# Kernel tuning notes

Hardware: AMD Instinct MI355X
Metric: run time of the kernel (lower is better)

The kernel has to match this reference:

```python
import jax, jax.numpy as jnp
import numpy as np

B, S, D, H = 256, 200, 256, 4
HD = D // H
R = 16  # HIE reduced rank (hardcoded in module)
EPS = 1e-12


def setup_inputs() -> dict:
    key = jax.random.key(0)
    ks = jax.random.split(key, 32)
    w = lambda k, sh: jax.random.normal(k, sh, jnp.float32) * 0.02
    inp = {
        'input_tensor': jax.random.normal(ks[0], (B, S, D), jnp.float32),
        'fusion_tensor': jax.random.normal(ks[1], (B, S, D), jnp.float32),
        'pos_tensor': jax.random.normal(ks[2], (B, S, D), jnp.float32),
        'attention_mask': jnp.zeros((B, 1, 1, S), jnp.float32),
        # projections (stored as (in, out); apply as x @ W + b)
        'Wv': w(ks[3], (D, D)), 'bv': w(ks[4], (D,)),
        'Wqf': w(ks[5], (D, D)), 'bqf': w(ks[6], (D,)),
        'Wkf': w(ks[7], (D, D)), 'bkf': w(ks[8], (D,)),
        'Wvf': w(ks[9], (D, D)), 'bvf': w(ks[10], (D,)),
        'Wqp': w(ks[11], (D, D)), 'bqp': w(ks[12], (D,)),
        'Wkp': w(ks[13], (D, D)), 'bkp': w(ks[14], (D,)),
        'Wvp': w(ks[15], (D, D)), 'bvp': w(ks[16], (D,)),
        # output dense + LayerNorm per branch
        'Wd': w(ks[17], (D, D)), 'bd': w(ks[18], (D,)),
        'g1': jnp.ones((D,), jnp.float32), 'b1': jnp.zeros((D,), jnp.float32),
        'Wfd': w(ks[19], (D, D)), 'bfd': w(ks[20], (D,)),
        'g2': jnp.ones((D,), jnp.float32), 'b2': jnp.zeros((D,), jnp.float32),
        'Wpd': w(ks[21], (D, D)), 'bpd': w(ks[22], (D,)),
        'g3': jnp.ones((D,), jnp.float32), 'b3': jnp.zeros((D,), jnp.float32),
        # HIE parameter (n, r)
        'Wr': jax.random.normal(ks[23], (S, R), jnp.float32),
    }
    return inp


def _heads(t):
    # (B,S,D) -> (B,H,S,HD)
    return t.reshape(B, S, H, HD).transpose(0, 2, 1, 3)


def _layernorm(x, g, b):
    m = jnp.mean(x, axis=-1, keepdims=True)
    v = jnp.mean((x - m) ** 2, axis=-1, keepdims=True)
    return (x - m) * jax.lax.rsqrt(v + EPS) * g + b


def _compute(resid, value_layer, scores, mask, Wd, bd, g, b):
    s = scores / np.sqrt(HD) + mask
    probs = jax.nn.softmax(s, axis=-1)  # (attn dropout = identity in eval)
    ctx = jnp.einsum('bhqk,bhkd->bhqd', probs, value_layer)
    ctx = ctx.transpose(0, 2, 1, 3).reshape(B, S, D)
    return _layernorm(ctx @ Wd + bd + resid, g, b)


def _hie(hX, hA, Wr):
    # reduce sequence dim, batched QR on (d, r) columns
    hr = jnp.einsum('bnd,nr->brd', hX, Wr)        # (B,R,D)
    Q, _ = jnp.linalg.qr(hr.transpose(0, 2, 1))   # (B,D,R), reduced
    pX = hX @ Q                                    # (B,S,R)
    pA = hA @ Q
    pAt = (pX * pA > 0).astype(pA.dtype) * pA      # indicator gate
    return jnp.einsum('bnr,bdr->bnd', pAt, Q)


def reference(input_tensor, fusion_tensor, pos_tensor, attention_mask,
              Wv, bv, Wqf, bqf, Wkf, bkf, Wvf, bvf, Wqp, bqp, Wkp, bkp,
              Wvp, bvp, Wd, bd, g1, b1, Wfd, bfd, g2, b2, Wpd, bpd, g3, b3, Wr):
    item_v = _heads(input_tensor @ Wv + bv)
    fq = _heads(fusion_tensor @ Wqf + bqf)
    fk = _heads(fusion_tensor @ Wkf + bkf)
    fv = _heads(fusion_tensor @ Wvf + bvf)
    pq = _heads(pos_tensor @ Wqp + bqp)
    pk = _heads(pos_tensor @ Wkp + bkp)
    pv = _heads(pos_tensor @ Wvp + bvp)

    item_scores = jnp.einsum('bhqd,bhkd->bhqk', fq, fk)
    pos_scores = jnp.einsum('bhqd,bhkd->bhqk', pq, pk)
    both_scores = item_scores + pos_scores

    h = _compute(input_tensor, item_v, both_scores, attention_mask, Wd, bd, g1, b1)
    hf = _compute(fusion_tensor, fv, item_scores, attention_mask, Wfd, bfd, g2, b2)
    hp = _compute(pos_tensor, pv, pos_scores, attention_mask, Wpd, bpd, g3, b3)

    h = h + _hie(h, hf, Wr)
    return (h, hf, hp)
```

## Files before the change

kernel.cpp:

```cpp
#include <hip/hip_runtime.h>


constexpr int B_ = 256, S_ = 200, D_ = 256, H_ = 4, R_ = 16;
constexpr int M_ = B_ * S_;
constexpr size_t BSD = (size_t)B_ * S_ * D_;

typedef __attribute__((ext_vector_type(8))) short bf16x8;
typedef __attribute__((ext_vector_type(4))) short bf16x4;
typedef __attribute__((ext_vector_type(4))) float f32x4;

#if __has_builtin(__builtin_amdgcn_mfma_f32_16x16x16bf16_1k)
#define MFMA16(A, B, C) __builtin_amdgcn_mfma_f32_16x16x16bf16_1k((A), (B), (C), 0, 0, 0)
#define HAVE_MFMA16 1
#else
#define HAVE_MFMA16 0
#endif

__device__ __forceinline__ float bf2f(unsigned short u) {
  union { unsigned int i; float f; } v; v.i = ((unsigned int)u) << 16; return v.f;
}
__device__ __forceinline__ unsigned short f2bf_rne(float f) {
  union { float f; unsigned int i; } v; v.f = f;
  unsigned int u = v.i;
  u += 0x7FFFu + ((u >> 16) & 1u);
  return (unsigned short)(u >> 16);
}
__device__ __forceinline__ void split8(const float* v, bf16x8& hi, bf16x8& lo) {
#pragma unroll
  for (int i = 0; i < 8; ++i) {
    unsigned short h = f2bf_rne(v[i]);
    hi[i] = (short)h;
    lo[i] = (short)f2bf_rne(v[i] - bf2f(h));
  }
}
__device__ __forceinline__ void unpack8(uint4 a, uint4 b, bf16x8& hi, bf16x8& lo) {
  union { bf16x8 v; unsigned int u[4]; } H, L;
  H.u[0] = (a.x & 0xffffu) | (a.y << 16);
  H.u[1] = (a.z & 0xffffu) | (a.w << 16);
  H.u[2] = (b.x & 0xffffu) | (b.y << 16);
  H.u[3] = (b.z & 0xffffu) | (b.w << 16);
  L.u[0] = (a.x >> 16) | (a.y & 0xffff0000u);
  L.u[1] = (a.z >> 16) | (a.w & 0xffff0000u);
  L.u[2] = (b.x >> 16) | (b.y & 0xffff0000u);
  L.u[3] = (b.z >> 16) | (b.w & 0xffff0000u);
  hi = H.v; lo = L.v;
}

struct GemmArgs {
  const float* X[7]; const float* bias[7]; float* Y[7];
  const float* resid[7]; const float* g[7]; const float* bvec[7];
  const unsigned short* stash;
};
struct WSplitArgs { const float* W[7]; };

__global__ __launch_bounds__(256) void split_w(WSplitArgs wa, unsigned short* stash)
{
  const int z = blockIdx.y;
  const int idx = blockIdx.x * 256 + threadIdx.x;
  const int k = idx >> 8, n = idx & 255;
  const float x = wa.W[z][idx];
  const unsigned short h = f2bf_rne(x);
  const unsigned short l = f2bf_rne(x - bf2f(h));
  const size_t o = (size_t)z * 131072 + (size_t)n * 256 + k;
  stash[o] = h;
  stash[o + 65536] = l;
}

template<int MODE>
__global__ __launch_bounds__(256, 2) void gemm_mfma(GemmArgs ga)
{
  __shared__ unsigned short lds[30720];
  unsigned short* Ah = lds;
  unsigned short* Al = Ah + 128 * 40;
  unsigned short* Bh = Al + 128 * 40;
  unsigned short* Bl = Bh + 256 * 40;
  const int t = threadIdx.x;
  const int z = blockIdx.y;
  const int m0 = blockIdx.x * 128;
  const float* __restrict__ X = ga.X[z];
  const float* __restrict__ bias = ga.bias[z];
  float* __restrict__ Y = ga.Y[z];
  const unsigned short* __restrict__ Wst = ga.stash + (size_t)z * 131072;
  const int w = t >> 6, lane = t & 63;
  const int wm = w >> 1, wn = w & 1;
  const int lrow = lane & 15;
  const int lk = (lane >> 4) << 3;
  const int rsub = (lane >> 4) << 2;

  f32x4 acc[4][8];
#pragma unroll
  for (int mf = 0; mf < 4; ++mf)
#pragma unroll
    for (int nf = 0; nf < 8; ++nf)
#pragma unroll
      for (int r = 0; r < 4; ++r) acc[mf][nf][r] = 0.f;

  for (int k0 = 0; k0 < 256; k0 += 32) {
#pragma unroll
    for (int i = 0; i < 2; ++i) {
      int c = t + i * 256;
      int r = c >> 2, c8 = (c & 3) << 3;
      float xv[8];
      *reinterpret_cast<float4*>(&xv[0]) =
          *reinterpret_cast<const float4*>(X + (size_t)(m0 + r) * 256 + k0 + c8);
      *reinterpret_cast<float4*>(&xv[4]) =
          *reinterpret_cast<const float4*>(X + (size_t)(m0 + r) * 256 + k0 + c8 + 4);
      bf16x8 hv, lv;
      split8(xv, hv, lv);
      *reinterpret_cast<bf16x8*>(&Ah[r * 40 + c8]) = hv;
      *reinterpret_cast<bf16x8*>(&Al[r * 40 + c8]) = lv;
    }
#pragma unroll
    for (int i = 0; i < 4; ++i) {
      int c = t + i * 256;
      int n = c >> 2, kc = (c & 3) << 3;
      *reinterpret_cast<uint4*>(&Bh[n * 40 + kc]) =
          *reinterpret_cast<const uint4*>(Wst + (size_t)n * 256 + k0 + kc);
      *reinterpret_cast<uint4*>(&Bl[n * 40 + kc]) =
          *reinterpret_cast<const uint4*>(Wst + 65536 + (size_t)n * 256 + k0 + kc);
    }
    __syncthreads();
    bf16x8 ah[4], al[4];
#pragma unroll
    for (int mf = 0; mf < 4; ++mf) {
      int r = wm * 64 + mf * 16 + lrow;
      ah[mf] = *reinterpret_cast<const bf16x8*>(&Ah[r * 40 + lk]);
      al[mf] = *reinterpret_cast<const bf16x8*>(&Al[r * 40 + lk]);
    }
#pragma unroll
    for (int nf = 0; nf < 8; ++nf) {
      int n = wn * 128 + nf * 16 + lrow;
      bf16x8 bh = *reinterpret_cast<const bf16x8*>(&Bh[n * 40 + lk]);
      bf16x8 bl = *reinterpret_cast<const bf16x8*>(&Bl[n * 40 + lk]);
#pragma unroll
      for (int mf = 0; mf < 4; ++mf) {
        acc[mf][nf] = __builtin_amdgcn_mfma_f32_16x16x32_bf16(ah[mf], bh, acc[mf][nf], 0, 0, 0);
        acc[mf][nf] = __builtin_amdgcn_mfma_f32_16x16x32_bf16(al[mf], bh, acc[mf][nf], 0, 0, 0);
        acc[mf][nf] = __builtin_amdgcn_mfma_f32_16x16x32_bf16(ah[mf], bl, acc[mf][nf], 0, 0, 0);
      }
    }
    __syncthreads();
  }

  if (MODE == 0) {
    unsigned int* Yu = (unsigned int*)Y;
#pragma unroll
    for (int nf = 0; nf < 8; ++nf) {
      const int coln = wn * 128 + nf * 16 + lrow;
      const float bb = bias[coln];
#pragma unroll
      for (int mf = 0; mf < 4; ++mf)
#pragma unroll
        for (int r = 0; r < 4; ++r) {
          const size_t row = (size_t)(m0 + wm * 64 + mf * 16 + rsub + r);
          float v = acc[mf][nf][r] + bb;
          unsigned short hh = f2bf_rne(v);
          unsigned short ll = f2bf_rne(v - bf2f(hh));
          Yu[row * 256 + coln] = (unsigned int)hh | ((unsigned int)ll << 16);
        }
    }
  } else {
    const float* __restrict__ resid = ga.resid[z];
    const float* __restrict__ gv = ga.g[z];
    const float* __restrict__ bv = ga.bvec[z];
    float s_[4][4], q_[4][4];
#pragma unroll
    for (int mf = 0; mf < 4; ++mf)
#pragma unroll
      for (int r = 0; r < 4; ++r) { s_[mf][r] = 0.f; q_[mf][r] = 0.f; }
#pragma unroll
    for (int nf = 0; nf < 8; ++nf) {
      const int coln = wn * 128 + nf * 16 + lrow;
      const float bb = bias[coln];
#pragma unroll
      for (int mf = 0; mf < 4; ++mf)
#pragma unroll
        for (int r = 0; r < 4; ++r) {
          const size_t row = (size_t)(m0 + wm * 64 + mf * 16 + rsub + r);
          float v = acc[mf][nf][r] + bb + resid[row * 256 + coln];
          acc[mf][nf][r] = v;
          s_[mf][r] += v;
          q_[mf][r] = fmaf(v, v, q_[mf][r]);
        }
    }
#pragma unroll
    for (int mf = 0; mf < 4; ++mf)
#pragma unroll
      for (int r = 0; r < 4; ++r) {
        float sv = s_[mf][r], qv = q_[mf][r];
        sv += __shfl_xor(sv, 1); qv += __shfl_xor(qv, 1);
        sv += __shfl_xor(sv, 2); qv += __shfl_xor(qv, 2);
        sv += __shfl_xor(sv, 4); qv += __shfl_xor(qv, 4);
        sv += __shfl_xor(sv, 8); qv += __shfl_xor(qv, 8);
        s_[mf][r] = sv; q_[mf][r] = qv;
      }
    __syncthreads();
    float* red = (float*)lds;
    if (lrow == 0) {
#pragma unroll
      for (int mf = 0; mf < 4; ++mf)
#pragma unroll
        for (int r = 0; r < 4; ++r) {
          int rl = wm * 64 + mf * 16 + rsub + r;
          red[rl * 4 + wn * 2 + 0] = s_[mf][r];
          red[rl * 4 + wn * 2 + 1] = q_[mf][r];
        }
    }
    __syncthreads();
#pragma unroll
    for (int mf = 0; mf < 4; ++mf)
#pragma unroll
      for (int r = 0; r < 4; ++r) {
        int rl = wm * 64 + mf * 16 + rsub + r;
        float st = red[rl * 4 + 0] + red[rl * 4 + 2];
        float qt = red[rl * 4 + 1] + red[rl * 4 + 3];
        float mean = st * (1.0f / 256.0f);
        float var = qt * (1.0f / 256.0f) - mean * mean;
        s_[mf][r] = mean;
        q_[mf][r] = rsqrtf(var + 1e-12f);
      }
#pragma unroll
    for (int nf = 0; nf < 8; ++nf) {
      const int coln = wn * 128 + nf * 16 + lrow;
      const float gg = gv[coln], be = bv[coln];
#pragma unroll
      for (int mf = 0; mf < 4; ++mf)
#pragma unroll
        for (int r = 0; r < 4; ++r) {
          const size_t row = (size_t)(m0 + wm * 64 + mf * 16 + rsub + r);
          Y[row * 256 + coln] = (acc[mf][nf][r] - s_[mf][r]) * q_[mf][r] * gg + be;
        }
    }
  }
}

__global__ __launch_bounds__(256) void attn_mfma(
    const unsigned int* __restrict__ Qf, const unsigned int* __restrict__ Kf,
    const unsigned int* __restrict__ Qp, const unsigned int* __restrict__ Kp,
    const unsigned int* __restrict__ Vi, const unsigned int* __restrict__ Vf,
    const unsigned int* __restrict__ Vp, const float* __restrict__ mask,
    float* __restrict__ Ch, float* __restrict__ Cf, float* __restrict__ Cp)
{
  __shared__ unsigned short su[21504];
  __shared__ float mt[32];
  __shared__ float emt[32];
  constexpr int KFH = 0,     KFL = 2816,  KPH = 5632,  KPL = 8448;
  constexpr int VIH = 11264, VIL = 13824, VFH = 16384, VPH = 18944;
  const int t = threadIdx.x;
  const int mtile = blockIdx.x, h = blockIdx.y, b = blockIdx.z;
  const int w = t >> 6, lane = t & 63, lg = lane >> 4, lm = lane & 15;
  const int mbase = mtile * 128 + w * 32;
  const bool wactive = (mbase < 200);
  const size_t bh = (size_t)b * 200 * 256 + (size_t)h * 64;

  bf16x8 qfh[2][2], qfl[2][2], qph[2][2], qpl[2][2];
#pragma unroll
  for (int mf2 = 0; mf2 < 2; ++mf2) {
    int gq = mbase + mf2 * 16 + lm; if (gq > 199) gq = 199;
    const size_t qb = bh + (size_t)gq * 256;
#pragma unroll
    for (int ks = 0; ks < 2; ++ks) {
      const size_t o = qb + ks * 32 + lg * 8;
      uint4 a = *reinterpret_cast<const uint4*>(Qf + o);
      uint4 bb = *reinterpret_cast<const uint4*>(Qf + o + 4);
      unpack8(a, bb, qfh[mf2][ks], qfl[mf2][ks]);
      a = *reinterpret_cast<const uint4*>(Qp + o);
      bb = *reinterpret_cast<const uint4*>(Qp + o + 4);
      unpack8(a, bb, qph[mf2][ks], qpl[mf2][ks]);
    }
  }

  f32x4 aH[4][2], aF[4][2], aP[4][2];
#pragma unroll
  for (int df = 0; df < 4; ++df)
#pragma unroll
    for (int mf2 = 0; mf2 < 2; ++mf2)
#pragma unroll
      for (int r = 0; r < 4; ++r) { aH[df][mf2][r] = 0.f; aF[df][mf2][r] = 0.f; aP[df][mf2][r] = 0.f; }
  float lH[2] = {0.f, 0.f}, lF[2] = {0.f, 0.f}, lP[2] = {0.f, 0.f};

  for (int kt = 0; kt < 200; kt += 32) {
#pragma unroll
    for (int i = 0; i < 2; ++i) {
      int idx = t + i * 256;
      const int pk = idx >> 8;
      const int rr = (idx >> 3) & 31;
      const int c8 = (idx & 7) << 3;
      int grow = kt + rr; if (grow > 199) grow = 199;
      const unsigned int* src = pk ? Kp : Kf;
      const size_t o = bh + (size_t)grow * 256 + c8;
      uint4 a = *reinterpret_cast<const uint4*>(src + o);
      uint4 bb = *reinterpret_cast<const uint4*>(src + o + 4);
      bf16x8 hv, lv;
      unpack8(a, bb, hv, lv);
      const int KH = pk ? KPH : KFH;
      const int KL = pk ? KPL : KFL;
      *reinterpret_cast<bf16x8*>(&su[KH + rr * 88 + c8]) = hv;
      *reinterpret_cast<bf16x8*>(&su[KL + rr * 88 + c8]) = lv;
    }
#pragma unroll
    for (int i = 0; i < 2; ++i) {
      int idx = t + i * 256;
      int d = idx & 63, kv4i = (idx >> 6) << 2;
      size_t rb[4];
#pragma unroll
      for (int j = 0; j < 4; ++j) {
        int grow = kt + kv4i + j; if (grow > 199) grow = 199;
        rb[j] = bh + (size_t)grow * 256 + d;
      }
      unsigned int u0 = Vi[rb[0]], u1 = Vi[rb[1]], u2 = Vi[rb[2]], u3 = Vi[rb[3]];
      ushort4 hv, lv;
      hv.x = (unsigned short)u0; hv.y = (unsigned short)u1;
      hv.z = (unsigned short)u2; hv.w = (unsigned short)u3;
      lv.x = (unsigned short)(u0 >> 16); lv.y = (unsigned short)(u1 >> 16);
      lv.z = (unsigned short)(u2 >> 16); lv.w = (unsigned short)(u3 >> 16);
      *reinterpret_cast<ushort4*>(&su[VIH + d * 40 + kv4i]) = hv;
      *reinterpret_cast<ushort4*>(&su[VIL + d * 40 + kv4i]) = lv;
      u0 = Vf[rb[0]]; u1 = Vf[rb[1]]; u2 = Vf[rb[2]]; u3 = Vf[rb[3]];
      hv.x = (unsigned short)u0; hv.y = (unsigned short)u1;
      hv.z = (unsigned short)u2; hv.w = (unsigned short)u3;
      *reinterpret_cast<ushort4*>(&su[VFH + d * 40 + kv4i]) = hv;
      u0 = Vp[rb[0]]; u1 = Vp[rb[1]]; u2 = Vp[rb[2]]; u3 = Vp[rb[3]];
      hv.x = (unsigned short)u0; hv.y = (unsigned short)u1;
      hv.z = (unsigned short)u2; hv.w = (unsigned short)u3;
      *reinterpret_cast<ushort4*>(&su[VPH + d * 40 + kv4i]) = hv;
    }
    if (t < 32) {
      const bool valid = (kt + t < 200);
      const float mj = valid ? mask[(size_t)b * 200 + kt + t] : -1e30f;
      mt[t] = mj;
      emt[t] = valid ? __expf(-mj) : 0.f;
    }
    __syncthreads();

    if (wactive) {
      f32x4 si[2][2], sp[2][2];
#pragma unroll
      for (int kvf = 0; kvf < 2; ++kvf)
#pragma unroll
        for (int mf2 = 0; mf2 < 2; ++mf2)
#pragma unroll
          for (int r = 0; r < 4; ++r) { si[kvf][mf2][r] = 0.f; sp[kvf][mf2][r] = 0.f; }
#pragma unroll
      for (int ks = 0; ks < 2; ++ks)
#pragma unroll
        for (int kvf = 0; kvf < 2; ++kvf) {
          bf16x8 kh = *reinterpret_cast<const bf16x8*>(&su[KFH + (kvf * 16 + lm) * 88 + ks * 32 + lg * 8]);
          bf16x8 kl = *reinterpret_cast<const bf16x8*>(&su[KFL + (kvf * 16 + lm) * 88 + ks * 32 + lg * 8]);
#pragma unroll
          for (int mf2 = 0; mf2 < 2; ++mf2) {
            si[kvf][mf2] = __builtin_amdgcn_mfma_f32_16x16x32_bf16(kh, qfh[mf2][ks], si[kvf][mf2], 0, 0, 0);
            si[kvf][mf2] = __builtin_amdgcn_mfma_f32_16x16x32_bf16(kl, qfh[mf2][ks], si[kvf][mf2], 0, 0, 0);
            si[kvf][mf2] = __builtin_amdgcn_mfma_f32_16x16x32_bf16(kh, qfl[mf2][ks], si[kvf][mf2], 0, 0, 0);
          }
          kh = *reinterpret_cast<const bf16x8*>(&su[KPH + (kvf * 16 + lm) * 88 + ks * 32 + lg * 8]);
          kl = *reinterpret_cast<const bf16x8*>(&su[KPL + (kvf * 16 + lm) * 88 + ks * 32 + lg * 8]);
#pragma unroll
          for (int mf2 = 0; mf2 < 2; ++mf2) {
            sp[kvf][mf2] = __builtin_amdgcn_mfma_f32_16x16x32_bf16(kh, qph[mf2][ks], sp[kvf][mf2], 0, 0, 0);
            sp[kvf][mf2] = __builtin_amdgcn_mfma_f32_16x16x32_bf16(kl, qph[mf2][ks], sp[kvf][mf2], 0, 0, 0);
            sp[kvf][mf2] = __builtin_amdgcn_mfma_f32_16x16x32_bf16(kh, qpl[mf2][ks], sp[kvf][mf2], 0, 0, 0);
          }
        }

      f32x4 ph[2][2], pf[2][2], pp[2][2];
      float4 mv[2], ev[2];
      mv[0] = *reinterpret_cast<const float4*>(&mt[lg * 4]);
      mv[1] = *reinterpret_cast<const float4*>(&mt[16 + lg * 4]);
      ev[0] = *reinterpret_cast<const float4*>(&emt[lg * 4]);
      ev[1] = *reinterpret_cast<const float4*>(&emt[16 + lg * 4]);
#pragma unroll
      for (int kvf = 0; kvf < 2; ++kvf)
#pragma unroll
        for (int mf2 = 0; mf2 < 2; ++mf2)
#pragma unroll
          for (int r = 0; r < 4; ++r) {
            float mj = (r == 0) ? mv[kvf].x : (r == 1) ? mv[kvf].y : (r == 2) ? mv[kvf].z : mv[kvf].w;
            float ej = (r == 0) ? ev[kvf].x : (r == 1) ? ev[kvf].y : (r == 2) ? ev[kvf].z : ev[kvf].w;
            float vF = __expf(fmaf(si[kvf][mf2][r], 0.125f, mj));
            float vP = __expf(fmaf(sp[kvf][mf2][r], 0.125f, mj));
            float vH = vF * vP * ej;
            pf[kvf][mf2][r] = vF; pp[kvf][mf2][r] = vP; ph[kvf][mf2][r] = vH;
            lF[mf2] += vF; lP[mf2] += vP; lH[mf2] += vH;
          }

#if HAVE_MFMA16
#pragma unroll
      for (int kvf = 0; kvf < 2; ++kvf) {
        bf16x4 bH[2], bL[2], bF[2], bP[2];
#pragma unroll
        for (int mf2 = 0; mf2 < 2; ++mf2) {
#pragma unroll
          for (int i = 0; i < 4; ++i) {
            float vH = ph[kvf][mf2][i];
            unsigned short hh = f2bf_rne(vH);
            bH[mf2][i] = (short)hh;
            bL[mf2][i] = (short)f2bf_rne(vH - bf2f(hh));
            bF[mf2][i] = (short)f2bf_rne(pf[kvf][mf2][i]);
            bP[mf2][i] = (short)f2bf_rne(pp[kvf][mf2][i]);
          }
        }
#pragma unroll
        for (int df = 0; df < 4; ++df) {
          const int rowb = (df * 16 + lm) * 40 + kvf * 16 + lg * 4;
          bf16x4 vih = *reinterpret_cast<const bf16x4*>(&su[VIH + rowb]);
          bf16x4 vil = *reinterpret_cast<const bf16x4*>(&su[VIL + rowb]);
          bf16x4 vfh = *reinterpret_cast<const bf16x4*>(&su[VFH + rowb]);
          bf16x4 vph = *reinterpret_cast<const bf16x4*>(&su[VPH + rowb]);
#pragma unroll
          for (int mf2 = 0; mf2 < 2; ++mf2) {
            aH[df][mf2] = MFMA16(vih, bH[mf2], aH[df][mf2]);
            aH[df][mf2] = MFMA16(vil, bH[mf2], aH[df][mf2]);
            aH[df][mf2] = MFMA16(vih, bL[mf2], aH[df][mf2]);
            aF[df][mf2] = MFMA16(vfh, bF[mf2], aF[df][mf2]);
            aP[df][mf2] = MFMA16(vph, bP[mf2], aP[df][mf2]);
          }
        }
      }
#else
#define PV3(P, VH, VL, ACC)                                                    \
      {                                                                        \
        bf16x8 Bh[2], Bl[2];                                                   \
        _Pragma("unroll")                                                      \
        for (int mf2 = 0; mf2 < 2; ++mf2) {                                    \
          _Pragma("unroll")                                                    \
          for (int i = 0; i < 8; ++i) {                                        \
            int src = ((((lg & 1) * 2 + (i >> 2)) << 4) | lm);                 \
            float t0 = __shfl(P[0][mf2][i & 3], src);                          \
            float t1 = __shfl(P[1][mf2][i & 3], src);                          \
            float v = (lg < 2) ? t0 : t1;                                      \
            unsigned short hh = f2bf_rne(v);                                   \
            Bh[mf2][i] = (short)hh;                                            \
            Bl[mf2][i] = (short)f2bf_rne(v - bf2f(hh));                        \
          }                                                                    \
        }                                                                      \
        _Pragma("unroll")                                                      \
        for (int df = 0; df < 4; ++df) {                                       \
          bf16x8 vh = *reinterpret_cast<const bf16x8*>(&su[VH + (df * 16 + lm) * 40 + lg * 8]); \
          bf16x8 vl = *reinterpret_cast<const bf16x8*>(&su[VL + (df * 16 + lm) * 40 + lg * 8]); \
          _Pragma("unroll")                                                    \
          for (int mf2 = 0; mf2 < 2; ++mf2) {                                  \
            ACC[df][mf2] = __builtin_amdgcn_mfma_f32_16x16x32_bf16(vh, Bh[mf2], ACC[df][mf2], 0, 0, 0); \
            ACC[df][mf2] = __builtin_amdgcn_mfma_f32_16x16x32_bf16(vl, Bh[mf2], ACC[df][mf2], 0, 0, 0); \
            ACC[df][mf2] = __builtin_amdgcn_mfma_f32_16x16x32_bf16(vh, Bl[mf2], ACC[df][mf2], 0, 0, 0); \
          }                                                                    \
        }                                                                      \
      }
#define PV1(P, VH, ACC)                                                        \
      {                                                                        \
        bf16x8 Bh[2];                                                          \
        _Pragma("unroll")                                                      \
        for (int mf2 = 0; mf2 < 2; ++mf2) {                                    \
          _Pragma("unroll")                                                    \
          for (int i = 0; i < 8; ++i) {                                        \
            int src = ((((lg & 1) * 2 + (i >> 2)) << 4) | lm);                 \
            float t0 = __shfl(P[0][mf2][i & 3], src);                          \
            float t1 = __shfl(P[1][mf2][i & 3], src);                          \
            float v = (lg < 2) ? t0 : t1;                                      \
            Bh[mf2][i] = (short)f2bf_rne(v);                                   \
          }                                                                    \
        }                                                                      \
        _Pragma("unroll")                                                      \
        for (int df = 0; df < 4; ++df) {                                       \
          bf16x8 vh = *reinterpret_cast<const bf16x8*>(&su[VH + (df * 16 + lm) * 40 + lg * 8]); \
          _Pragma("unroll")                                                    \
          for (int mf2 = 0; mf2 < 2; ++mf2)                                    \
            ACC[df][mf2] = __builtin_amdgcn_mfma_f32_16x16x32_bf16(vh, Bh[mf2], ACC[df][mf2], 0, 0, 0); \
        }                                                                      \
      }
      PV3(ph, VIH, VIL, aH)
      PV1(pf, VFH, aF)
      PV1(pp, VPH, aP)
#undef PV3
#undef PV1
#endif
    }
    __syncthreads();
  }

#pragma unroll
  for (int mf2 = 0; mf2 < 2; ++mf2) {
    lH[mf2] += __shfl_xor(lH[mf2], 16); lH[mf2] += __shfl_xor(lH[mf2], 32);
    lF[mf2] += __shfl_xor(lF[mf2], 16); lF[mf2] += __shfl_xor(lF[mf2], 32);
    lP[mf2] += __shfl_xor(lP[mf2], 16); lP[mf2] += __shfl_xor(lP[mf2], 32);
  }

#pragma unroll
  for (int mf2 = 0; mf2 < 2; ++mf2) {
    int gq = mbase + mf2 * 16 + lm;
    if (gq < 200) {
      const size_t base = bh + (size_t)gq * 256;
      const float iH = 1.f / lH[mf2], iF = 1.f / lF[mf2], iP = 1.f / lP[mf2];
#pragma unroll
      for (int df = 0; df < 4; ++df) {
        float4 o;
        o.x = aH[df][mf2][0] * iH; o.y = aH[df][mf2][1] * iH;
        o.z = aH[df][mf2][2] * iH; o.w = aH[df][mf2][3] * iH;
        *reinterpret_cast<float4*>(Ch + base + df * 16 + lg * 4) = o;
        o.x = aF[df][mf2][0] * iF; o.y = aF[df][mf2][1] * iF;
        o.z = aF[df][mf2][2] * iF; o.w = aF[df][mf2][3] * iF;
        *reinterpret_cast<float4*>(Cf + base + df * 16 + lg * 4) = o;
        o.x = aP[df][mf2][0] * iP; o.y = aP[df][mf2][1] * iP;
        o.z = aP[df][mf2][2] * iP; o.w = aP[df][mf2][3] * iP;
        *reinterpret_cast<float4*>(Cp + base + df * 16 + lg * 4) = o;
      }
    }
  }
}

__global__ __launch_bounds__(256) void hie_hr_kernel(
    const float* __restrict__ h, const float* __restrict__ Wr, float* __restrict__ hr)
{
  __shared__ float wrs[3200];
  const int b = blockIdx.x, t = threadIdx.x;
  for (int i = t; i < 3200; i += 256) wrs[i] = Wr[i];
  __syncthreads();
  double acc[16];
#pragma unroll
  for (int r = 0; r < 16; ++r) acc[r] = 0.0;
  const float* hb = h + (size_t)b * 200 * 256;
  for (int n = 0; n < 200; ++n) {
    float hv = hb[(size_t)n * 256 + t];
#pragma unroll
    for (int r = 0; r < 16; ++r) acc[r] += (double)(hv * wrs[n * 16 + r]);
  }
#pragma unroll
  for (int r = 0; r < 16; ++r) hr[((size_t)b * 16 + r) * 256 + t] = (float)acc[r];
}

__global__ __launch_bounds__(256) void hie_qr_kernel(
    const float* __restrict__ hr, float* __restrict__ Qg)
{
  __shared__ float Qs[16][256];
  __shared__ double red[4];
  const int b = blockIdx.x, t = threadIdx.x;
  const int wid = t >> 6, lane = t & 63;
  const float* A = hr + (size_t)b * 4096;
#pragma unroll 1
  for (int j = 0; j < 16; ++j) {
    double v = (double)A[j * 256 + t];
#pragma unroll 1
    for (int i = 0; i < j; ++i) {
      float qi = Qs[i][t];
      double p = (double)qi * v;
#pragma unroll
      for (int off = 32; off; off >>= 1) p += __shfl_xor(p, off);
      if (lane == 0) red[wid] = p;
      __syncthreads();
      double dot = red[0] + red[1] + red[2] + red[3];
      __syncthreads();
      v -= dot * (double)qi;
    }
    double nn = v * v;
#pragma unroll
    for (int off = 32; off; off >>= 1) nn += __shfl_xor(nn, off);
    if (lane == 0) red[wid] = nn;
    __syncthreads();
    double nrm = sqrt(red[0] + red[1] + red[2] + red[3]);
    __syncthreads();
    float qv = (float)(v / nrm);
    Qs[j][t] = qv;
    Qg[(size_t)b * 4096 + j * 256 + t] = qv;
    __syncthreads();
  }
}

__global__ __launch_bounds__(256) void hie_pxgate(
    const float* __restrict__ hX, const float* __restrict__ hA,
    const float* __restrict__ Qg, float* __restrict__ patp)
{
  __shared__ float Qs[16][260];
  __shared__ float ha[16][260];
  __shared__ float hbx[16][260];
  const int ch = blockIdx.x, b = blockIdx.y, t = threadIdx.x;
  const int chunk = ch * 16;
  for (int i = t; i < 4096; i += 256) Qs[i >> 8][i & 255] = Qg[(size_t)b * 4096 + i];
#pragma unroll
  for (int i = 0; i < 4; ++i) {
    int c = t + i * 256;
    int rr = c >> 6, c4 = (c & 63) << 2;
    int n = chunk + rr;
    if (n < 200) {
      *reinterpret_cast<float4*>(&ha[rr][c4]) =
          *reinterpret_cast<const float4*>(hX + ((size_t)b * 200 + n) * 256 + c4);
      *reinterpret_cast<float4*>(&hbx[rr][c4]) =
          *reinterpret_cast<const float4*>(hA + ((size_t)b * 200 + n) * 256 + c4);
    }
  }
  __syncthreads();
  const int nl = t >> 4, r = t & 15;
  int n = chunk + nl;
  if (n < 200) {
    double ax = 0.0, aa = 0.0;
#pragma unroll
    for (int d4 = 0; d4 < 256; d4 += 4) {
      float4 qv = *reinterpret_cast<const float4*>(&Qs[r][d4]);
      float4 hv = *reinterpret_cast<const float4*>(&ha[nl][d4]);
      ax += (double)(hv.x * qv.x + hv.y * qv.y + hv.z * qv.z + hv.w * qv.w);
      hv = *reinterpret_cast<const float4*>(&hbx[nl][d4]);
      aa += (double)(hv.x * qv.x + hv.y * qv.y + hv.z * qv.z + hv.w * qv.w);
    }
    float px = (float)ax, pa = (float)aa;
    patp[((size_t)b * 200 + n) * 16 + r] = (px * pa > 0.0f) ? pa : 0.0f;
  }
}

__global__ __launch_bounds__(256) void hie_final_kernel(
    const float* __restrict__ h, const float* __restrict__ pat,
    const float* __restrict__ Qg, float* __restrict__ outp)
{
  __shared__ float Qs[16][260];
  __shared__ float pt[16][16];
  const int ch = blockIdx.x, b = blockIdx.y, t = threadIdx.x;
  const int chunk = ch * 16;
  for (int i = t; i < 4096; i += 256) Qs[i >> 8][i & 255] = Qg[(size_t)b * 4096 + i];
  const int nl = t >> 4, r = t & 15;
  {
    int n = chunk + nl;
    pt[nl][r] = (n < 200) ? pat[((size_t)b * 200 + n) * 16 + r] : 0.0f;
  }
  __syncthreads();
#pragma unroll 1
  for (int j = 0; j < 16; ++j) {
    int n = chunk + j;
    if (n >= 200) break;
    float acc = h[((size_t)b * 200 + n) * 256 + t];
#pragma unroll
    for (int rr = 0; rr < 16; ++rr) acc = fmaf(pt[j][rr], Qs[rr][t], acc);
    outp[((size_t)b * 200 + n) * 256 + t] = acc;
  }
}

__global__ void diag_kernel(float* out, float val, int n) {
  int i = blockIdx.x * 256 + threadIdx.x;
  if (i < n) out[i] = (i == 0) ? val : 0.0f;
}

extern "C" void kernel_launch(void* const* d_in, const int* in_sizes, int n_in,
                              void* d_out, int out_size, void* d_ws, size_t ws_size,
                              hipStream_t stream)
{
  (void)in_sizes; (void)n_in;
  const float* input  = (const float*)d_in[0];
  const float* fusion = (const float*)d_in[1];
  const float* pos    = (const float*)d_in[2];
  const float* mask   = (const float*)d_in[3];
  const float* Wv  = (const float*)d_in[4];  const float* bv  = (const float*)d_in[5];
  const float* Wqf = (const float*)d_in[6];  const float* bqf = (const float*)d_in[7];
  const float* Wkf = (const float*)d_in[8];  const float* bkf = (const float*)d_in[9];
  const float* Wvf = (const float*)d_in[10]; const float* bvf = (const float*)d_in[11];
  const float* Wqp = (const float*)d_in[12]; const float* bqp = (const float*)d_in[13];
  const float* Wkp = (const float*)d_in[14]; const float* bkp = (const float*)d_in[15];
  const float* Wvp = (const float*)d_in[16]; const float* bvp = (const float*)d_in[17];
  const float* Wd  = (const float*)d_in[18]; const float* bd  = (const float*)d_in[19];
  const float* g1  = (const float*)d_in[20]; const float* b1  = (const float*)d_in[21];
  const float* Wfd = (const float*)d_in[22]; const float* bfd = (const float*)d_in[23];
  const float* g2  = (const float*)d_in[24]; const float* b2  = (const float*)d_in[25];
  const float* Wpd = (const float*)d_in[26]; const float* bpd = (const float*)d_in[27];
  const float* g3  = (const float*)d_in[28]; const float* b3  = (const float*)d_in[29];
  const float* Wr  = (const float*)d_in[30];

  const size_t required = 7 * BSD * 4;
  if (ws_size < required) {
    diag_kernel<<<(out_size + 255) / 256, 256, 0, stream>>>(
        (float*)d_out, (float)(ws_size >> 20), out_size);
    return;
  }

  float* W0 = (float*)d_ws;
  float* O0 = (float*)d_out;
  float* O1 = O0 + BSD;
  float* O2 = O0 + 2 * BSD;
  float* s_fq = W0;
  float* s_fk = W0 + BSD;
  float* s_pq = W0 + 2 * BSD;
  float* s_pk = W0 + 3 * BSD;
  float* s_iv = W0 + 4 * BSD;
  float* s_fv = W0 + 5 * BSD;
  float* s_pv = W0 + 6 * BSD;
  float* hrb  = W0;
  float* Qb   = W0 + 1048576;
  float* patb = W0 + 2097152;
  unsigned short* stash1 = (unsigned short*)d_out;
  unsigned short* stash2 = (unsigned short*)(W0 + 4 * 1048576);

  dim3 Blk(256);

  WSplitArgs w7;
  w7.W[0] = Wqf; w7.W[1] = Wkf; w7.W[2] = Wqp; w7.W[3] = Wkp;
  w7.W[4] = Wv;  w7.W[5] = Wvf; w7.W[6] = Wvp;
  split_w<<<dim3(256, 7), Blk, 0, stream>>>(w7, stash1);

  GemmArgs pa = {};
  pa.X[0] = fusion; pa.bias[0] = bqf; pa.Y[0] = s_fq;
  pa.X[1] = fusion; pa.bias[1] = bkf; pa.Y[1] = s_fk;
  pa.X[2] = pos;    pa.bias[2] = bqp; pa.Y[2] = s_pq;
  pa.X[3] = pos;    pa.bias[3] = bkp; pa.Y[3] = s_pk;
  pa.X[4] = input;  pa.bias[4] = bv;  pa.Y[4] = s_iv;
  pa.X[5] = fusion; pa.bias[5] = bvf; pa.Y[5] = s_fv;
  pa.X[6] = pos;    pa.bias[6] = bvp; pa.Y[6] = s_pv;
  pa.stash = stash1;
  gemm_mfma<0><<<dim3(M_ / 128, 7), Blk, 0, stream>>>(pa);

  attn_mfma<<<dim3(2, H_, B_), Blk, 0, stream>>>(
      (const unsigned int*)s_fq, (const unsigned int*)s_fk,
      (const unsigned int*)s_pq, (const unsigned int*)s_pk,
      (const unsigned int*)s_iv, (const unsigned int*)s_fv,
      (const unsigned int*)s_pv, mask, O0, O1, O2);

  WSplitArgs w3;
  w3.W[0] = Wd; w3.W[1] = Wfd; w3.W[2] = Wpd;
  split_w<<<dim3(256, 3), Blk, 0, stream>>>(w3, stash2);

  GemmArgs da = {};
  da.X[0] = O0; da.bias[0] = bd;  da.Y[0] = O0; da.resid[0] = input;  da.g[0] = g1; da.bvec[0] = b1;
  da.X[1] = O1; da.bias[1] = bfd; da.Y[1] = O1; da.resid[1] = fusion; da.g[1] = g2; da.bvec[1] = b2;
  da.X[2] = O2; da.bias[2] = bpd; da.Y[2] = O2; da.resid[2] = pos;    da.g[2] = g3; da.bvec[2] = b3;
  da.stash = stash2;
  gemm_mfma<1><<<dim3(M_ / 128, 3), Blk, 0, stream>>>(da);

  hie_hr_kernel<<<B_, Blk, 0, stream>>>(O0, Wr, hrb);
  hie_qr_kernel<<<B_, Blk, 0, stream>>>(hrb, Qb);
  hie_pxgate<<<dim3(13, B_), Blk, 0, stream>>>(O0, O1, Qb, patb);
  hie_final_kernel<<<dim3(13, B_), Blk, 0, stream>>>(O0, patb, Qb, O0);
}
```

Before: 738.8 us.

## Use packed bf16 conversion, raise MFMA priority, and fuse HIE kernels

Replaces the manual round-to-nearest bf16 hi/lo splitting with the hardware v_cvt_pk_bf16_f32 instruction in the GEMM input staging, the GEMM epilogue and the attention P conversion. It also adds s_setprio around the MFMA blocks in attention. The four HIE kernels are merged into two: the sequence reduction is fused with the QR, and the gate is fused with the final projection. This removes intermediate global buffers and launches and reuses the staged h rows from LDS. The hardware conversion's rounding may differ slightly from the software RNE on edge cases such as NaN.

```diff
diff --git a/kernel.cpp b/kernel.cpp
--- a/kernel.cpp
+++ b/kernel.cpp
@@ -19,19 +19,36 @@
 __device__ __forceinline__ float bf2f(unsigned short u) {
   union { unsigned int i; float f; } v; v.i = ((unsigned int)u) << 16; return v.f;
 }
+__device__ __forceinline__ float bits2f(unsigned int u) {
+  union { unsigned int i; float f; } v; v.i = u; return v.f;
+}
 __device__ __forceinline__ unsigned short f2bf_rne(float f) {
   union { float f; unsigned int i; } v; v.f = f;
   unsigned int u = v.i;
   u += 0x7FFFu + ((u >> 16) & 1u);
   return (unsigned short)(u >> 16);
 }
-__device__ __forceinline__ void split8(const float* v, bf16x8& hi, bf16x8& lo) {
-#pragma unroll
-  for (int i = 0; i < 8; ++i) {
-    unsigned short h = f2bf_rne(v[i]);
-    hi[i] = (short)h;
-    lo[i] = (short)f2bf_rne(v[i] - bf2f(h));
-  }
+__device__ __forceinline__ unsigned int cvt_pk_bf16(float a, float b) {
+  unsigned int r;
+  asm("v_cvt_pk_bf16_f32 %0, %1, %2" : "=v"(r) : "v"(a), "v"(b));
+  return r;
+}
+__device__ __forceinline__ void split8_pk(const float* v, bf16x8& hi, bf16x8& lo) {
+  union { bf16x8 x; unsigned int u[4]; } H, L;
+#pragma unroll
+  for (int i = 0; i < 4; ++i) {
+    unsigned int h2 = cvt_pk_bf16(v[2 * i], v[2 * i + 1]);
+    H.u[i] = h2;
+    float h0 = bits2f(h2 << 16);
+    float h1 = bits2f(h2 & 0xffff0000u);
+    L.u[i] = cvt_pk_bf16(v[2 * i] - h0, v[2 * i + 1] - h1);
+  }
+  hi = H.x; lo = L.x;
+}
+__device__ __forceinline__ unsigned int pack_hl(float v) {
+  unsigned int h2 = cvt_pk_bf16(v, v);
+  float hf = bits2f(h2 << 16);
+  return cvt_pk_bf16(v, v - hf);
 }
 __device__ __forceinline__ void unpack8(uint4 a, uint4 b, bf16x8& hi, bf16x8& lo) {
   union { bf16x8 v; unsigned int u[4]; } H, L;
@@ -106,7 +123,7 @@
       *reinterpret_cast<float4*>(&xv[4]) =
           *reinterpret_cast<const float4*>(X + (size_t)(m0 + r) * 256 + k0 + c8 + 4);
       bf16x8 hv, lv;
-      split8(xv, hv, lv);
+      split8_pk(xv, hv, lv);
       *reinterpret_cast<bf16x8*>(&Ah[r * 40 + c8]) = hv;
       *reinterpret_cast<bf16x8*>(&Al[r * 40 + c8]) = lv;
     }
@@ -153,10 +170,7 @@
 #pragma unroll
         for (int r = 0; r < 4; ++r) {
           const size_t row = (size_t)(m0 + wm * 64 + mf * 16 + rsub + r);
-          float v = acc[mf][nf][r] + bb;
-          unsigned short hh = f2bf_rne(v);
-          unsigned short ll = f2bf_rne(v - bf2f(hh));
-          Yu[row * 256 + coln] = (unsigned int)hh | ((unsigned int)ll << 16);
+          Yu[row * 256 + coln] = pack_hl(acc[mf][nf][r] + bb);
         }
     }
   } else {
@@ -341,6 +355,7 @@
         for (int mf2 = 0; mf2 < 2; ++mf2)
 #pragma unroll
           for (int r = 0; r < 4; ++r) { si[kvf][mf2][r] = 0.f; sp[kvf][mf2][r] = 0.f; }
+      __builtin_amdgcn_s_setprio(1);
 #pragma unroll
       for (int ks = 0; ks < 2; ++ks)
 #pragma unroll
@@ -362,6 +377,7 @@
             sp[kvf][mf2] = __builtin_amdgcn_mfma_f32_16x16x32_bf16(kh, qpl[mf2][ks], sp[kvf][mf2], 0, 0, 0);
           }
         }
+      __builtin_amdgcn_s_setprio(0);
 
       f32x4 ph[2][2], pf[2][2], pp[2][2];
       float4 mv[2], ev[2];
@@ -390,16 +406,22 @@
         bf16x4 bH[2], bL[2], bF[2], bP[2];
 #pragma unroll
         for (int mf2 = 0; mf2 < 2; ++mf2) {
-#pragma unroll
-          for (int i = 0; i < 4; ++i) {
-            float vH = ph[kvf][mf2][i];
-            unsigned short hh = f2bf_rne(vH);
-            bH[mf2][i] = (short)hh;
-            bL[mf2][i] = (short)f2bf_rne(vH - bf2f(hh));
-            bF[mf2][i] = (short)f2bf_rne(pf[kvf][mf2][i]);
-            bP[mf2][i] = (short)f2bf_rne(pp[kvf][mf2][i]);
-          }
+          union { bf16x4 x; unsigned int u[2]; } BH, BL, BF, BP;
+          BH.u[0] = cvt_pk_bf16(ph[kvf][mf2][0], ph[kvf][mf2][1]);
+          BH.u[1] = cvt_pk_bf16(ph[kvf][mf2][2], ph[kvf][mf2][3]);
+          float h0 = bits2f(BH.u[0] << 16);
+          float h1 = bits2f(BH.u[0] & 0xffff0000u);
+          float h2 = bits2f(BH.u[1] << 16);
+          float h3 = bits2f(BH.u[1] & 0xffff0000u);
+          BL.u[0] = cvt_pk_bf16(ph[kvf][mf2][0] - h0, ph[kvf][mf2][1] - h1);
+          BL.u[1] = cvt_pk_bf16(ph[kvf][mf2][2] - h2, ph[kvf][mf2][3] - h3);
+          BF.u[0] = cvt_pk_bf16(pf[kvf][mf2][0], pf[kvf][mf2][1]);
+          BF.u[1] = cvt_pk_bf16(pf[kvf][mf2][2], pf[kvf][mf2][3]);
+          BP.u[0] = cvt_pk_bf16(pp[kvf][mf2][0], pp[kvf][mf2][1]);
+          BP.u[1] = cvt_pk_bf16(pp[kvf][mf2][2], pp[kvf][mf2][3]);
+          bH[mf2] = BH.x; bL[mf2] = BL.x; bF[mf2] = BF.x; bP[mf2] = BP.x;
         }
+        __builtin_amdgcn_s_setprio(1);
 #pragma unroll
         for (int df = 0; df < 4; ++df) {
           const int rowb = (df * 16 + lm) * 40 + kvf * 16 + lg * 4;
@@ -416,6 +438,7 @@
             aP[df][mf2] = MFMA16(vph, bP[mf2], aP[df][mf2]);
           }
         }
+        __builtin_amdgcn_s_setprio(0);
       }
 #else
 #define PV3(P, VH, VL, ACC)                                                    \
@@ -456,7 +479,7 @@
             int src = ((((lg & 1) * 2 + (i >> 2)) << 4) | lm);                 \
             float t0 = __shfl(P[0][mf2][i & 3], src);                          \
             float t1 = __shfl(P[1][mf2][i & 3], src);                          \
-            float v = (lg < 2) ? t0 : t1;                                      \
+            float v = (lg < 2) ? t0 : t1;                                     \
             Bh[mf2][i] = (short)f2bf_rne(v);                                   \
           }                                                                    \
         }                                                                      \
@@ -508,11 +531,14 @@
   }
 }
 
-__global__ __launch_bounds__(256) void hie_hr_kernel(
-    const float* __restrict__ h, const float* __restrict__ Wr, float* __restrict__ hr)
+__global__ __launch_bounds__(256) void hie_hrqr(
+    const float* __restrict__ h, const float* __restrict__ Wr, float* __restrict__ Qg)
 {
   __shared__ float wrs[3200];
+  __shared__ float A[16][256];
+  __shared__ double red[4];
   const int b = blockIdx.x, t = threadIdx.x;
+  const int wid = t >> 6, lane = t & 63;
   for (int i = t; i < 3200; i += 256) wrs[i] = Wr[i];
   __syncthreads();
   double acc[16];
@@ -525,23 +551,14 @@
     for (int r = 0; r < 16; ++r) acc[r] += (double)(hv * wrs[n * 16 + r]);
   }
 #pragma unroll
-  for (int r = 0; r < 16; ++r) hr[((size_t)b * 16 + r) * 256 + t] = (float)acc[r];
-}
-
-__global__ __launch_bounds__(256) void hie_qr_kernel(
-    const float* __restrict__ hr, float* __restrict__ Qg)
-{
-  __shared__ float Qs[16][256];
-  __shared__ double red[4];
-  const int b = blockIdx.x, t = threadIdx.x;
-  const int wid = t >> 6, lane = t & 63;
-  const float* A = hr + (size_t)b * 4096;
+  for (int r = 0; r < 16; ++r) A[r][t] = (float)acc[r];
+  __syncthreads();
 #pragma unroll 1
   for (int j = 0; j < 16; ++j) {
-    double v = (double)A[j * 256 + t];
+    double v = (double)A[j][t];
 #pragma unroll 1
     for (int i = 0; i < j; ++i) {
-      float qi = Qs[i][t];
+      float qi = A[i][t];
       double p = (double)qi * v;
 #pragma unroll
       for (int off = 32; off; off >>= 1) p += __shfl_xor(p, off);
@@ -559,19 +576,20 @@
     double nrm = sqrt(red[0] + red[1] + red[2] + red[3]);
     __syncthreads();
     float qv = (float)(v / nrm);
-    Qs[j][t] = qv;
+    A[j][t] = qv;
     Qg[(size_t)b * 4096 + j * 256 + t] = qv;
     __syncthreads();
   }
 }
 
-__global__ __launch_bounds__(256) void hie_pxgate(
+__global__ __launch_bounds__(256) void hie_tail(
     const float* __restrict__ hX, const float* __restrict__ hA,
-    const float* __restrict__ Qg, float* __restrict__ patp)
+    const float* __restrict__ Qg, float* __restrict__ outp)
 {
   __shared__ float Qs[16][260];
   __shared__ float ha[16][260];
   __shared__ float hbx[16][260];
+  __shared__ float pt[16][16];
   const int ch = blockIdx.x, b = blockIdx.y, t = threadIdx.x;
   const int chunk = ch * 16;
   for (int i = t; i < 4096; i += 256) Qs[i >> 8][i & 255] = Qg[(size_t)b * 4096 + i];
@@ -589,42 +607,30 @@
   }
   __syncthreads();
   const int nl = t >> 4, r = t & 15;
-  int n = chunk + nl;
-  if (n < 200) {
-    double ax = 0.0, aa = 0.0;
-#pragma unroll
-    for (int d4 = 0; d4 < 256; d4 += 4) {
-      float4 qv = *reinterpret_cast<const float4*>(&Qs[r][d4]);
-      float4 hv = *reinterpret_cast<const float4*>(&ha[nl][d4]);
-      ax += (double)(hv.x * qv.x + hv.y * qv.y + hv.z * qv.z + hv.w * qv.w);
-      hv = *reinterpret_cast<const float4*>(&hbx[nl][d4]);
-      aa += (double)(hv.x * qv.x + hv.y * qv.y + hv.z * qv.z + hv.w * qv.w);
-    }
-    float px = (float)ax, pa = (float)aa;
-    patp[((size_t)b * 200 + n) * 16 + r] = (px * pa > 0.0f) ? pa : 0.0f;
-  }
-}
-
-__global__ __launch_bounds__(256) void hie_final_kernel(
-    const float* __restrict__ h, const float* __restrict__ pat,
-    const float* __restrict__ Qg, float* __restrict__ outp)
-{
-  __shared__ float Qs[16][260];
-  __shared__ float pt[16][16];
-  const int ch = blockIdx.x, b = blockIdx.y, t = threadIdx.x;
-  const int chunk = ch * 16;
-  for (int i = t; i < 4096; i += 256) Qs[i >> 8][i & 255] = Qg[(size_t)b * 4096 + i];
-  const int nl = t >> 4, r = t & 15;
   {
     int n = chunk + nl;
-    pt[nl][r] = (n < 200) ? pat[((size_t)b * 200 + n) * 16 + r] : 0.0f;
+    float gate = 0.f;
+    if (n < 200) {
+      double ax = 0.0, aa = 0.0;
+#pragma unroll
+      for (int d4 = 0; d4 < 256; d4 += 4) {
+        float4 qv = *reinterpret_cast<const float4*>(&Qs[r][d4]);
+        float4 hv = *reinterpret_cast<const float4*>(&ha[nl][d4]);
+        ax += (double)(hv.x * qv.x + hv.y * qv.y + hv.z * qv.z + hv.w * qv.w);
+        hv = *reinterpret_cast<const float4*>(&hbx[nl][d4]);
+        aa += (double)(hv.x * qv.x + hv.y * qv.y + hv.z * qv.z + hv.w * qv.w);
+      }
+      float px = (float)ax, pa = (float)aa;
+      gate = (px * pa > 0.0f) ? pa : 0.0f;
+    }
+    pt[nl][r] = gate;
   }
   __syncthreads();
 #pragma unroll 1
   for (int j = 0; j < 16; ++j) {
     int n = chunk + j;
     if (n >= 200) break;
-    float acc = h[((size_t)b * 200 + n) * 256 + t];
+    float acc = ha[j][t];
 #pragma unroll
     for (int rr = 0; rr < 16; ++rr) acc = fmaf(pt[j][rr], Qs[rr][t], acc);
     outp[((size_t)b * 200 + n) * 256 + t] = acc;
@@ -678,9 +684,7 @@
   float* s_iv = W0 + 4 * BSD;
   float* s_fv = W0 + 5 * BSD;
   float* s_pv = W0 + 6 * BSD;
-  float* hrb  = W0;
   float* Qb   = W0 + 1048576;
-  float* patb = W0 + 2097152;
   unsigned short* stash1 = (unsigned short*)d_out;
   unsigned short* stash2 = (unsigned short*)(W0 + 4 * 1048576);
 
@@ -719,8 +723,6 @@
   da.stash = stash2;
   gemm_mfma<1><<<dim3(M_ / 128, 3), Blk, 0, stream>>>(da);
 
-  hie_hr_kernel<<<B_, Blk, 0, stream>>>(O0, Wr, hrb);
-  hie_qr_kernel<<<B_, Blk, 0, stream>>>(hrb, Qb);
-  hie_pxgate<<<dim3(13, B_), Blk, 0, stream>>>(O0, O1, Qb, patb);
-  hie_final_kernel<<<dim3(13, B_), Blk, 0, stream>>>(O0, patb, Qb, O0);
-}
+  hie_hrqr<<<B_, Blk, 0, stream>>>(O0, Wr, Qb);
+  hie_tail<<<dim3(13, B_), Blk, 0, stream>>>(O0, O1, Qb, O0);
+}
```

New measurement: 691.1 us. 6.5% less time.
